# Kernel optimization log

Hardware: AMD Instinct MI355X
Metric: run time of the kernel (lower is better)

The kernel has to match this reference:

```python
import jax, jax.numpy as jnp
import numpy as np

# Dimensions: SASA-style local self-attention, 7x7 window, 8 groups (heads)
B, CIN, H, W = 4, 256, 64, 64
COUT, K, PAD, STRIDE, DIL, G = 256, 7, 3, 1, 1, 8
CG = COUT // G  # channels per group


def setup_inputs() -> dict:
    key = jax.random.key(0)
    k1, k2, k3, k4, k5, k6 = jax.random.split(key, 6)
    s = 1.0 / np.sqrt(CIN // G)  # fan-in scaling like torch conv init
    return {
        "inputs": jax.random.normal(k1, (B, CIN, H, W), jnp.float32),
        "w_q": jax.random.normal(k2, (G, CG, CIN // G), jnp.float32) * s,
        "w_k": jax.random.normal(k3, (G, CG, CIN // G), jnp.float32) * s,
        "w_v": jax.random.normal(k4, (G, CG, CIN // G), jnp.float32) * s,
        "row_emb": jax.random.normal(k5, (COUT // 2, K), jnp.float32),
        "col_emb": jax.random.normal(k6, (COUT // 2, K), jnp.float32),
    }


def _proj(x, w):
    # grouped 1x1 conv: x [B,CIN,H,W], w [G, CG, CIN/G] -> [B,G,CG,H,W]
    xg = x.reshape(B, G, CIN // G, H, W)
    return jnp.einsum('goc,bgchw->bgohw', w, xg)


def _out_hw():
    ho = (H + 2 * PAD - DIL * (K - 1) - 1) // STRIDE + 1
    wo = (W + 2 * PAD - DIL * (K - 1) - 1) // STRIDE + 1
    return ho, wo


def _patches(x):
    # im2col matching torch.nn.Unfold ordering (kh slow, kw fast)
    # x [B,G,CG,H,W] -> [B,G,CG,K*K,Ho,Wo]
    ho, wo = _out_hw()
    xp = jnp.pad(x, ((0, 0), (0, 0), (0, 0), (PAD, PAD), (PAD, PAD)))
    pats = [
        xp[..., i * DIL: i * DIL + (ho - 1) * STRIDE + 1: STRIDE,
              j * DIL: j * DIL + (wo - 1) * STRIDE + 1: STRIDE]
        for i in range(K) for j in range(K)
    ]
    return jnp.stack(pats, axis=3)


def reference(inputs, w_q, w_k, w_v, row_emb, col_emb):
    ho, wo = _out_hw()
    # queries: 1x1 conv then unfold with kernel 1 / stride -> just strided subsample
    q = _proj(inputs, w_q)[..., ::STRIDE, ::STRIDE]          # [B,G,CG,Ho,Wo]
    kk = _patches(_proj(inputs, w_k))                         # [B,G,CG,K2,Ho,Wo]
    vv = _patches(_proj(inputs, w_v))                         # [B,G,CG,K2,Ho,Wo]
    # relative row/col embeddings, concatenated along channels, split per group
    emb_row = jnp.broadcast_to(row_emb[:, :, None], (COUT // 2, K, K))
    emb_col = jnp.broadcast_to(col_emb[:, None, :], (COUT // 2, K, K))
    emb = jnp.concatenate([emb_row, emb_col], axis=0).reshape(G, CG, K * K)
    # attention logits: per-position dot of query with (key + embedding)
    logits = jnp.einsum('bgchw,bgckhw->bgkhw', q, kk + emb[None, :, :, :, None, None])
    attn = jax.nn.softmax(logits, axis=2)                     # softmax over K*K window
    out = jnp.einsum('bgckhw,bgkhw->bgchw', vv, attn)
    return out.reshape(B, COUT, ho, wo)
```

## Files before the change

kernel.cpp:

```cpp
#include <hip/hip_runtime.h>
#include <hip/hip_bf16.h>
#include <hip/hip_fp16.h>

#define TS   16
#define HS   22
#define HP   484
#define KDW  18
#define KK   7
#define K2   49

typedef _Float16 h2 __attribute__((ext_vector_type(2)));
union U32H { unsigned u; h2 h; __half2 p; };

__device__ __forceinline__ h2 pkrtz(float a, float b) {
    auto r = __builtin_amdgcn_cvt_pkrtz(a, b);
    union { decltype(r) i; h2 o; } c; c.i = r;
    return c.o;
}
__device__ __forceinline__ float dot2(h2 a, h2 b, float c) {
#if __has_builtin(__builtin_amdgcn_fdot2)
    return __builtin_amdgcn_fdot2(a, b, c, false);
#else
    return fmaf((float)a.x, (float)b.x, fmaf((float)a.y, (float)b.y, c));
#endif
}
__device__ __forceinline__ float dot2u(unsigned wu, h2 b, float c) {
    U32H w; w.u = wu; return dot2(w.h, b, c);
}
__device__ __forceinline__ float pswap(float v) {
#if __has_builtin(__builtin_amdgcn_mov_dpp)
    int j = __builtin_amdgcn_mov_dpp(__float_as_int(v), 0xB1, 0xF, 0xF, true);
    return __int_as_float(j);
#else
    return __shfl_xor(v, 1, 64);
#endif
}

__global__ __attribute__((amdgpu_flat_work_group_size(512, 512), amdgpu_waves_per_eu(4, 4)))
void sasa_fused_kernel(const float* __restrict__ x,
                       const float* __restrict__ wq,
                       const float* __restrict__ wk,
                       const float* __restrict__ wv,
                       const float* __restrict__ row_emb,
                       const float* __restrict__ col_emb,
                       float* __restrict__ out)
{
    __shared__ h2       s_w[1536];
    __shared__ float    s_emb[224];
    __shared__ unsigned s_ku[HP * KDW];
    __shared__ unsigned s_vu[HP * KDW];

    const int tid = threadIdx.x;

    const int lin  = blockIdx.x + (blockIdx.y << 2) + (blockIdx.z << 4);
    const int xcd  = lin & 7;
    const int slot = lin >> 3;
    const int zg   = xcd + ((slot >> 4) << 3);
    const int sp   = slot & 15;
    const int b    = zg >> 3;
    const int g    = zg & 7;
    const int y0   = (sp >> 2) * TS;
    const int x0   = (sp & 3) * TS;

    const float* xg = x + (size_t)(b * 256 + g * 32) * 4096;

    const int hh0 = (tid >= HP) ? 1 : 0;
    const int hp0 = tid - (hh0 ? HP : 0);
    const int hy0 = hp0 / HS, hx0 = hp0 - hy0 * HS;
    const int gy0 = y0 + hy0 - 3, gx0 = x0 + hx0 - 3;
    const bool ok0 = ((unsigned)gy0 < 64u) && ((unsigned)gx0 < 64u);

    const int hp1 = tid + 28;
    const int hy1 = hp1 / HS, hx1 = hp1 - hy1 * HS;
    const int gy1 = y0 + hy1 - 3, gx1 = x0 + hx1 - 3;
    const bool it1v = (tid < 2 * HP - 512);
    const bool ok1 = it1v && ((unsigned)gy1 < 64u) && ((unsigned)gx1 < 64u);

    float xr0[32], xr1[32];
    #pragma unroll
    for (int ci = 0; ci < 32; ++ci) { xr0[ci] = 0.f; xr1[ci] = 0.f; }
    if (ok0) {
        const float* xp = xg + gy0 * 64 + gx0;
        #pragma unroll
        for (int ci = 0; ci < 32; ++ci) xr0[ci] = xp[ci * 4096];
    }
    if (ok1) {
        const float* xp = xg + gy1 * 64 + gx1;
        #pragma unroll
        for (int ci = 0; ci < 32; ++ci) xr1[ci] = xp[ci * 4096];
    }

    {
        const int cp  = tid & 15;
        const int cog = tid >> 4;
        const int hh  = cog >> 4;
        const int co  = cog & 15;
        const int di  = (hh * 16 + cp) * 16 + co;
        const float2* wk2 = (const float2*)(wk + g * 1024);
        const float2* wv2 = (const float2*)(wv + g * 1024);
        const float2* wq2 = (const float2*)(wq + g * 1024);
        float2 a = wk2[tid]; s_w[di]        = pkrtz(a.x, a.y);
        float2 v = wv2[tid]; s_w[512 + di]  = pkrtz(v.x, v.y);
        float2 q = wq2[tid]; s_w[1024 + di] = pkrtz(q.x, q.y);
    }
    if (tid < 224) {
        int c = tid / KK, t = tid - c * KK;
        s_emb[tid] = (g < 4) ? row_emb[(g * 32 + c) * KK + t]
                             : col_emb[((g - 4) * 32 + c) * KK + t];
    }
    __syncthreads();

    {
        h2 xv2[16];
        #pragma unroll
        for (int cp = 0; cp < 16; ++cp) xv2[cp] = pkrtz(xr0[2 * cp], xr0[2 * cp + 1]);
        float accK[16], accV[16];
        #pragma unroll
        for (int c = 0; c < 16; ++c) { accK[c] = 0.f; accV[c] = 0.f; }
        const h2* wkp = s_w + hh0 * 256;
        const h2* wvp = s_w + 512 + hh0 * 256;
        #pragma unroll
        for (int cp = 0; cp < 16; ++cp) {
            h2 xv = xv2[cp];
            const uint4* wkr = (const uint4*)(wkp + cp * 16);
            const uint4* wvr = (const uint4*)(wvp + cp * 16);
            uint4 kw[4] = { wkr[0], wkr[1], wkr[2], wkr[3] };
            uint4 vw[4] = { wvr[0], wvr[1], wvr[2], wvr[3] };
            const unsigned* kwu = (const unsigned*)kw;
            const unsigned* vwu = (const unsigned*)vw;
            #pragma unroll
            for (int co = 0; co < 16; ++co) {
                accK[co] = dot2u(kwu[co], xv, accK[co]);
                accV[co] = dot2u(vwu[co], xv, accV[co]);
            }
        }
        unsigned* dk = s_ku + hp0 * KDW + hh0 * 8;
        unsigned* dv = s_vu + hp0 * KDW + hh0 * 8;
        #pragma unroll
        for (int j = 0; j < 4; ++j) {
            U32H a0, a1, b0, b1;
            a0.h = pkrtz(accK[4 * j],     accK[4 * j + 1]);
            a1.h = pkrtz(accK[4 * j + 2], accK[4 * j + 3]);
            b0.h = pkrtz(accV[4 * j],     accV[4 * j + 1]);
            b1.h = pkrtz(accV[4 * j + 2], accV[4 * j + 3]);
            ((uint2*)dk)[j] = make_uint2(a0.u, a1.u);
            ((uint2*)dv)[j] = make_uint2(b0.u, b1.u);
        }
    }
    if (it1v) {
        h2 xv2[16];
        #pragma unroll
        for (int cp = 0; cp < 16; ++cp) xv2[cp] = pkrtz(xr1[2 * cp], xr1[2 * cp + 1]);
        float accK[16], accV[16];
        #pragma unroll
        for (int c = 0; c < 16; ++c) { accK[c] = 0.f; accV[c] = 0.f; }
        const h2* wkp = s_w + 256;
        const h2* wvp = s_w + 512 + 256;
        #pragma unroll
        for (int cp = 0; cp < 16; ++cp) {
            h2 xv = xv2[cp];
            const uint4* wkr = (const uint4*)(wkp + cp * 16);
            const uint4* wvr = (const uint4*)(wvp + cp * 16);
            uint4 kw[4] = { wkr[0], wkr[1], wkr[2], wkr[3] };
            uint4 vw[4] = { wvr[0], wvr[1], wvr[2], wvr[3] };
            const unsigned* kwu = (const unsigned*)kw;
            const unsigned* vwu = (const unsigned*)vw;
            #pragma unroll
            for (int co = 0; co < 16; ++co) {
                accK[co] = dot2u(kwu[co], xv, accK[co]);
                accV[co] = dot2u(vwu[co], xv, accV[co]);
            }
        }
        unsigned* dk = s_ku + hp1 * KDW + 8;
        unsigned* dv = s_vu + hp1 * KDW + 8;
        #pragma unroll
        for (int j = 0; j < 4; ++j) {
            U32H a0, a1, b0, b1;
            a0.h = pkrtz(accK[4 * j],     accK[4 * j + 1]);
            a1.h = pkrtz(accK[4 * j + 2], accK[4 * j + 3]);
            b0.h = pkrtz(accV[4 * j],     accV[4 * j + 1]);
            b1.h = pkrtz(accV[4 * j + 2], accV[4 * j + 3]);
            ((uint2*)dk)[j] = make_uint2(a0.u, a1.u);
            ((uint2*)dv)[j] = make_uint2(b0.u, b1.u);
        }
    }

    const int p  = tid >> 1;
    const int h  = tid & 1;
    const int tx = p & 15, ty = p >> 4;
    const int yy = y0 + ty, xx = x0 + tx;
    float accQ[16];
    #pragma unroll
    for (int c = 0; c < 16; ++c) accQ[c] = 0.f;
    {
        const float* xp = xg + yy * 64 + xx;
        h2 xv2[16];
        #pragma unroll
        for (int cp = 0; cp < 16; ++cp)
            xv2[cp] = pkrtz(xp[(2 * cp) * 4096], xp[(2 * cp + 1) * 4096]);
        const h2* wqp = s_w + 1024 + h * 256;
        #pragma unroll
        for (int cp = 0; cp < 16; ++cp) {
            h2 xv = xv2[cp];
            const uint4* wqr = (const uint4*)(wqp + cp * 16);
            uint4 qw[4] = { wqr[0], wqr[1], wqr[2], wqr[3] };
            const unsigned* qwu = (const unsigned*)qw;
            #pragma unroll
            for (int co = 0; co < 16; ++co)
                accQ[co] = dot2u(qwu[co], xv, accQ[co]);
        }
    }

    float qe[KK];
    #pragma unroll
    for (int t = 0; t < KK; ++t) {
        float a = 0.f;
        #pragma unroll
        for (int c = 0; c < 16; ++c)
            a = fmaf(accQ[c], s_emb[(h * 16 + c) * KK + t], a);
        qe[t] = a + 0.f;
    }
    #pragma unroll
    for (int t = 0; t < KK; ++t)
        qe[t] += pswap(qe[t]);

    h2 q2[8];
    #pragma unroll
    for (int j = 0; j < 8; ++j) q2[j] = pkrtz(accQ[2 * j], accQ[2 * j + 1]);

    __syncthreads();

    const int rowsel = (g < 4) ? 1 : 0;

    float lg[K2];
    const unsigned* kb = s_ku + h * 8;
    #pragma unroll
    for (int tp = 0; tp < 24; ++tp) {
        const int t0 = 2 * tp, t1 = t0 + 1;
        const int ki0 = t0 / KK, kj0 = t0 - ki0 * KK;
        const int ki1 = t1 / KK, kj1 = t1 - ki1 * KK;
        const uint2* kp0 = (const uint2*)(kb + ((ty + ki0) * HS + tx + kj0) * KDW);
        const uint2* kp1 = (const uint2*)(kb + ((ty + ki1) * HS + tx + kj1) * KDW);
        uint2 a0 = kp0[0], a1 = kp0[1], a2 = kp0[2], a3 = kp0[3];
        uint2 b0 = kp1[0], b1 = kp1[1], b2 = kp1[2], b3 = kp1[3];
        float p0 = 0.f, p1 = 0.f;
        p0 = dot2u(a0.x, q2[0], p0);  p1 = dot2u(b0.x, q2[0], p1);
        p0 = dot2u(a0.y, q2[1], p0);  p1 = dot2u(b0.y, q2[1], p1);
        p0 = dot2u(a1.x, q2[2], p0);  p1 = dot2u(b1.x, q2[2], p1);
        p0 = dot2u(a1.y, q2[3], p0);  p1 = dot2u(b1.y, q2[3], p1);
        p0 = dot2u(a2.x, q2[4], p0);  p1 = dot2u(b2.x, q2[4], p1);
        p0 = dot2u(a2.y, q2[5], p0);  p1 = dot2u(b2.y, q2[5], p1);
        p0 = dot2u(a3.x, q2[6], p0);  p1 = dot2u(b3.x, q2[6], p1);
        p0 = dot2u(a3.y, q2[7], p0);  p1 = dot2u(b3.y, q2[7], p1);
        lg[t0] = p0 + pswap(p0) + (rowsel ? qe[ki0] : qe[kj0]);
        lg[t1] = p1 + pswap(p1) + (rowsel ? qe[ki1] : qe[kj1]);
    }
    {
        const uint2* kp = (const uint2*)(kb + ((ty + 6) * HS + tx + 6) * KDW);
        uint2 a0 = kp[0], a1 = kp[1], a2 = kp[2], a3 = kp[3];
        float p0 = 0.f;
        p0 = dot2u(a0.x, q2[0], p0); p0 = dot2u(a0.y, q2[1], p0);
        p0 = dot2u(a1.x, q2[2], p0); p0 = dot2u(a1.y, q2[3], p0);
        p0 = dot2u(a2.x, q2[4], p0); p0 = dot2u(a2.y, q2[5], p0);
        p0 = dot2u(a3.x, q2[6], p0); p0 = dot2u(a3.y, q2[7], p0);
        lg[48] = p0 + pswap(p0) + qe[6];
    }

    float m0 = lg[0], m1 = lg[1], m2 = lg[2], m3 = lg[3];
    #pragma unroll
    for (int t = 4; t < 48; t += 4) {
        m0 = fmaxf(m0, lg[t]);
        m1 = fmaxf(m1, lg[t + 1]);
        m2 = fmaxf(m2, lg[t + 2]);
        m3 = fmaxf(m3, lg[t + 3]);
    }
    const float mx = fmaxf(fmaxf(m0, m1), fmaxf(m2, fmaxf(m3, lg[48])));

    float s0 = 0.f, s1 = 0.f, s2 = 0.f, s3 = 0.f;
    #pragma unroll
    for (int t = 0; t < K2; ++t) {
        float pe = __expf(lg[t] - mx);
        lg[t] = pe;
        if ((t & 3) == 0) s0 += pe;
        else if ((t & 3) == 1) s1 += pe;
        else if ((t & 3) == 2) s2 += pe;
        else s3 += pe;
    }
    const float s = (s0 + s1) + (s2 + s3);

    __half2 o2[8];
    #pragma unroll
    for (int j = 0; j < 8; ++j) o2[j] = __float2half2_rn(0.f);

    const unsigned* vb = s_vu + h * 8;
    #pragma unroll
    for (int tp = 0; tp < 24; ++tp) {
        const int t0 = 2 * tp, t1 = t0 + 1;
        const int ki0 = t0 / KK, kj0 = t0 - ki0 * KK;
        const int ki1 = t1 / KK, kj1 = t1 - ki1 * KK;
        const uint2* vp0 = (const uint2*)(vb + ((ty + ki0) * HS + tx + kj0) * KDW);
        const uint2* vp1 = (const uint2*)(vb + ((ty + ki1) * HS + tx + kj1) * KDW);
        uint2 a0 = vp0[0], a1 = vp0[1], a2 = vp0[2], a3 = vp0[3];
        uint2 b0 = vp1[0], b1 = vp1[1], b2 = vp1[2], b3 = vp1[3];
        const __half2 pe0 = __float2half2_rn(lg[t0]);
        const __half2 pe1 = __float2half2_rn(lg[t1]);
        U32H c0, c1, c2, c3, c4, c5, c6, c7;
        c0.u = a0.x; c1.u = a0.y; c2.u = a1.x; c3.u = a1.y;
        c4.u = a2.x; c5.u = a2.y; c6.u = a3.x; c7.u = a3.y;
        o2[0] = __hfma2(c0.p, pe0, o2[0]);
        o2[1] = __hfma2(c1.p, pe0, o2[1]);
        o2[2] = __hfma2(c2.p, pe0, o2[2]);
        o2[3] = __hfma2(c3.p, pe0, o2[3]);
        o2[4] = __hfma2(c4.p, pe0, o2[4]);
        o2[5] = __hfma2(c5.p, pe0, o2[5]);
        o2[6] = __hfma2(c6.p, pe0, o2[6]);
        o2[7] = __hfma2(c7.p, pe0, o2[7]);
        c0.u = b0.x; c1.u = b0.y; c2.u = b1.x; c3.u = b1.y;
        c4.u = b2.x; c5.u = b2.y; c6.u = b3.x; c7.u = b3.y;
        o2[0] = __hfma2(c0.p, pe1, o2[0]);
        o2[1] = __hfma2(c1.p, pe1, o2[1]);
        o2[2] = __hfma2(c2.p, pe1, o2[2]);
        o2[3] = __hfma2(c3.p, pe1, o2[3]);
        o2[4] = __hfma2(c4.p, pe1, o2[4]);
        o2[5] = __hfma2(c5.p, pe1, o2[5]);
        o2[6] = __hfma2(c6.p, pe1, o2[6]);
        o2[7] = __hfma2(c7.p, pe1, o2[7]);
    }
    {
        const uint2* vp = (const uint2*)(vb + ((ty + 6) * HS + tx + 6) * KDW);
        uint2 a0 = vp[0], a1 = vp[1], a2 = vp[2], a3 = vp[3];
        const __half2 pe0 = __float2half2_rn(lg[48]);
        U32H c0, c1, c2, c3, c4, c5, c6, c7;
        c0.u = a0.x; c1.u = a0.y; c2.u = a1.x; c3.u = a1.y;
        c4.u = a2.x; c5.u = a2.y; c6.u = a3.x; c7.u = a3.y;
        o2[0] = __hfma2(c0.p, pe0, o2[0]);
        o2[1] = __hfma2(c1.p, pe0, o2[1]);
        o2[2] = __hfma2(c2.p, pe0, o2[2]);
        o2[3] = __hfma2(c3.p, pe0, o2[3]);
        o2[4] = __hfma2(c4.p, pe0, o2[4]);
        o2[5] = __hfma2(c5.p, pe0, o2[5]);
        o2[6] = __hfma2(c6.p, pe0, o2[6]);
        o2[7] = __hfma2(c7.p, pe0, o2[7]);
    }

    const float inv = 1.0f / s;
    float* op = out + (size_t)(b * 256 + g * 32 + h * 16) * 4096 + yy * 64 + xx;
    #pragma unroll
    for (int j = 0; j < 8; ++j) {
        float2 f = __half22float2(o2[j]);
        op[(2 * j) * 4096]     = f.x * inv;
        op[(2 * j + 1) * 4096] = f.y * inv;
    }
}

extern "C" void kernel_launch(void* const* d_in, const int* in_sizes, int n_in,
                              void* d_out, int out_size, void* d_ws, size_t ws_size,
                              hipStream_t stream) {
    const float* x       = (const float*)d_in[0];
    const float* wq      = (const float*)d_in[1];
    const float* wk      = (const float*)d_in[2];
    const float* wv      = (const float*)d_in[3];
    const float* row_emb = (const float*)d_in[4];
    const float* col_emb = (const float*)d_in[5];
    float* out = (float*)d_out;

    dim3 grid(4, 4, 32);
    dim3 block(512);
    sasa_fused_kernel<<<grid, block, 0, stream>>>(x, wq, wk, wv, row_emb, col_emb, out);
}
```

Measured before the change: 49.87 us.

## Compute halo K/V projections with MFMA 16x16x32 f16 instead of dot2 loops

Replaces the per-thread fdot2 loops that project halo pixels into key and value channels with wavefront-level MFMA f16 matrix multiplies over tiles of 16 halo pixels. Weights are gathered once into B-fragments, and each wave loops over tiles and scatters results into the shared K/V buffers. The halo input loads also move from upfront register prefetch into the tile loop. This cuts VALU work but loses the early load latency hiding and writes LDS with scattered half-word stores.

```diff
diff --git a/kernel.cpp b/kernel.cpp
--- a/kernel.cpp
+++ b/kernel.cpp
@@ -9,7 +9,9 @@
 #define KK   7
 #define K2   49
 
-typedef _Float16 h2 __attribute__((ext_vector_type(2)));
+typedef _Float16 h2   __attribute__((ext_vector_type(2)));
+typedef _Float16 f16x8 __attribute__((ext_vector_type(8)));
+typedef float    f32x4 __attribute__((ext_vector_type(4)));
 union U32H { unsigned u; h2 h; __half2 p; };
 
 __device__ __forceinline__ h2 pkrtz(float a, float b) {
@@ -64,32 +66,6 @@
 
     const float* xg = x + (size_t)(b * 256 + g * 32) * 4096;
 
-    const int hh0 = (tid >= HP) ? 1 : 0;
-    const int hp0 = tid - (hh0 ? HP : 0);
-    const int hy0 = hp0 / HS, hx0 = hp0 - hy0 * HS;
-    const int gy0 = y0 + hy0 - 3, gx0 = x0 + hx0 - 3;
-    const bool ok0 = ((unsigned)gy0 < 64u) && ((unsigned)gx0 < 64u);
-
-    const int hp1 = tid + 28;
-    const int hy1 = hp1 / HS, hx1 = hp1 - hy1 * HS;
-    const int gy1 = y0 + hy1 - 3, gx1 = x0 + hx1 - 3;
-    const bool it1v = (tid < 2 * HP - 512);
-    const bool ok1 = it1v && ((unsigned)gy1 < 64u) && ((unsigned)gx1 < 64u);
-
-    float xr0[32], xr1[32];
-    #pragma unroll
-    for (int ci = 0; ci < 32; ++ci) { xr0[ci] = 0.f; xr1[ci] = 0.f; }
-    if (ok0) {
-        const float* xp = xg + gy0 * 64 + gx0;
-        #pragma unroll
-        for (int ci = 0; ci < 32; ++ci) xr0[ci] = xp[ci * 4096];
-    }
-    if (ok1) {
-        const float* xp = xg + gy1 * 64 + gx1;
-        #pragma unroll
-        for (int ci = 0; ci < 32; ++ci) xr1[ci] = xp[ci * 4096];
-    }
-
     {
         const int cp  = tid & 15;
         const int cog = tid >> 4;
@@ -111,77 +87,68 @@
     __syncthreads();
 
     {
-        h2 xv2[16];
-        #pragma unroll
-        for (int cp = 0; cp < 16; ++cp) xv2[cp] = pkrtz(xr0[2 * cp], xr0[2 * cp + 1]);
-        float accK[16], accV[16];
-        #pragma unroll
-        for (int c = 0; c < 16; ++c) { accK[c] = 0.f; accV[c] = 0.f; }
-        const h2* wkp = s_w + hh0 * 256;
-        const h2* wvp = s_w + 512 + hh0 * 256;
-        #pragma unroll
-        for (int cp = 0; cp < 16; ++cp) {
-            h2 xv = xv2[cp];
-            const uint4* wkr = (const uint4*)(wkp + cp * 16);
-            const uint4* wvr = (const uint4*)(wvp + cp * 16);
-            uint4 kw[4] = { wkr[0], wkr[1], wkr[2], wkr[3] };
-            uint4 vw[4] = { wvr[0], wvr[1], wvr[2], wvr[3] };
-            const unsigned* kwu = (const unsigned*)kw;
-            const unsigned* vwu = (const unsigned*)vw;
-            #pragma unroll
-            for (int co = 0; co < 16; ++co) {
-                accK[co] = dot2u(kwu[co], xv, accK[co]);
-                accV[co] = dot2u(vwu[co], xv, accV[co]);
-            }
-        }
-        unsigned* dk = s_ku + hp0 * KDW + hh0 * 8;
-        unsigned* dv = s_vu + hp0 * KDW + hh0 * 8;
+        const int lane = tid & 63;
+        const int wid  = tid >> 6;
+        const int lrow = lane & 15;
+        const int lgrp = lane >> 4;
+
+        f16x8 bk0, bk1, bv0, bv1;
         #pragma unroll
         for (int j = 0; j < 4; ++j) {
-            U32H a0, a1, b0, b1;
-            a0.h = pkrtz(accK[4 * j],     accK[4 * j + 1]);
-            a1.h = pkrtz(accK[4 * j + 2], accK[4 * j + 3]);
-            b0.h = pkrtz(accV[4 * j],     accV[4 * j + 1]);
-            b1.h = pkrtz(accV[4 * j + 2], accV[4 * j + 3]);
-            ((uint2*)dk)[j] = make_uint2(a0.u, a1.u);
-            ((uint2*)dv)[j] = make_uint2(b0.u, b1.u);
+            const int cp = lgrp * 4 + j;
+            h2 pk0 = s_w[(0 * 16 + cp) * 16 + lrow];
+            h2 pk1 = s_w[(1 * 16 + cp) * 16 + lrow];
+            h2 pv0 = s_w[512 + (0 * 16 + cp) * 16 + lrow];
+            h2 pv1 = s_w[512 + (1 * 16 + cp) * 16 + lrow];
+            bk0[2 * j] = pk0.x; bk0[2 * j + 1] = pk0.y;
+            bk1[2 * j] = pk1.x; bk1[2 * j + 1] = pk1.y;
+            bv0[2 * j] = pv0.x; bv0[2 * j + 1] = pv0.y;
+            bv1[2 * j] = pv1.x; bv1[2 * j + 1] = pv1.y;
         }
-    }
-    if (it1v) {
-        h2 xv2[16];
-        #pragma unroll
-        for (int cp = 0; cp < 16; ++cp) xv2[cp] = pkrtz(xr1[2 * cp], xr1[2 * cp + 1]);
-        float accK[16], accV[16];
-        #pragma unroll
-        for (int c = 0; c < 16; ++c) { accK[c] = 0.f; accV[c] = 0.f; }
-        const h2* wkp = s_w + 256;
-        const h2* wvp = s_w + 512 + 256;
-        #pragma unroll
-        for (int cp = 0; cp < 16; ++cp) {
-            h2 xv = xv2[cp];
-            const uint4* wkr = (const uint4*)(wkp + cp * 16);
-            const uint4* wvr = (const uint4*)(wvp + cp * 16);
-            uint4 kw[4] = { wkr[0], wkr[1], wkr[2], wkr[3] };
-            uint4 vw[4] = { wvr[0], wvr[1], wvr[2], wvr[3] };
-            const unsigned* kwu = (const unsigned*)kw;
-            const unsigned* vwu = (const unsigned*)vw;
+
+        _Float16* sk16 = (_Float16*)s_ku;
+        _Float16* sv16 = (_Float16*)s_vu;
+        const f32x4 zero = {0.f, 0.f, 0.f, 0.f};
+
+        #pragma unroll 1
+        for (int t = wid; t < 31; t += 8) {
+            const int hp = t * 16 + lrow;
+            f16x8 a;
+            bool valid = false;
+            int gy = 0, gx = 0;
+            if (hp < HP) {
+                const int hy = hp / HS, hx = hp - hy * HS;
+                gy = y0 + hy - 3; gx = x0 + hx - 3;
+                valid = ((unsigned)gy < 64u) && ((unsigned)gx < 64u);
+            }
+            if (valid) {
+                const float* xp = xg + gy * 64 + gx + (size_t)(lgrp * 8) * 4096;
+                #pragma unroll
+                for (int i2 = 0; i2 < 4; ++i2) {
+                    h2 pr = pkrtz(xp[(2 * i2) * 4096], xp[(2 * i2 + 1) * 4096]);
+                    a[2 * i2] = pr.x; a[2 * i2 + 1] = pr.y;
+                }
+            } else {
+                #pragma unroll
+                for (int i = 0; i < 8; ++i) a[i] = (_Float16)0.f;
+            }
+
+            f32x4 dk0 = __builtin_amdgcn_mfma_f32_16x16x32_f16(a, bk0, zero, 0, 0, 0);
+            f32x4 dk1 = __builtin_amdgcn_mfma_f32_16x16x32_f16(a, bk1, zero, 0, 0, 0);
+            f32x4 dv0 = __builtin_amdgcn_mfma_f32_16x16x32_f16(a, bv0, zero, 0, 0, 0);
+            f32x4 dv1 = __builtin_amdgcn_mfma_f32_16x16x32_f16(a, bv1, zero, 0, 0, 0);
+
             #pragma unroll
-            for (int co = 0; co < 16; ++co) {
-                accK[co] = dot2u(kwu[co], xv, accK[co]);
-                accV[co] = dot2u(vwu[co], xv, accV[co]);
+            for (int r = 0; r < 4; ++r) {
+                const int hpo = t * 16 + lgrp * 4 + r;
+                if (hpo < HP) {
+                    const int base = hpo * 36;
+                    sk16[base + lrow]      = (_Float16)dk0[r];
+                    sk16[base + 16 + lrow] = (_Float16)dk1[r];
+                    sv16[base + lrow]      = (_Float16)dv0[r];
+                    sv16[base + 16 + lrow] = (_Float16)dv1[r];
+                }
             }
-        }
-        unsigned* dk = s_ku + hp1 * KDW + 8;
-        unsigned* dv = s_vu + hp1 * KDW + 8;
-        #pragma unroll
-        for (int j = 0; j < 4; ++j) {
-            U32H a0, a1, b0, b1;
-            a0.h = pkrtz(accK[4 * j],     accK[4 * j + 1]);
-            a1.h = pkrtz(accK[4 * j + 2], accK[4 * j + 3]);
-            b0.h = pkrtz(accV[4 * j],     accV[4 * j + 1]);
-            b1.h = pkrtz(accV[4 * j + 2], accV[4 * j + 3]);
-            ((uint2*)dk)[j] = make_uint2(a0.u, a1.u);
-            ((uint2*)dv)[j] = make_uint2(b0.u, b1.u);
         }
     }
 
```

Measured after the change: 40.06 us, median of 2. 1.25x faster.
